# Kernel optimization log

Measured on AMD Instinct MI355X. Metric: run time of the kernel, lower is better.

## Reference

```python
import jax, jax.numpy as jnp
import numpy as np

N = 38333          # poi_len == number of graph nodes (forced by fc_layer input dim)
E = 38333 * 32     # edges, avg degree 32
VOCAB = 400 + 38333 + 1083   # cat_len + poi_len + user_len = 39816
EMB = (128 - 3) // 2         # 62
IN_DIM = EMB * 2 + 3         # 127
SLOPE = 0.01                 # LeakyReLU default negative_slope


def setup_inputs() -> dict:
    key = jax.random.key(0)
    ks = jax.random.split(key, 20)
    ids = jax.random.randint(ks[0], (N, 2), 0, VOCAB).astype(jnp.float32)
    feats = jax.random.uniform(ks[1], (N, 3), dtype=jnp.float32)
    x = jnp.concatenate([ids, feats], axis=1)                      # [N,5]
    edge_index = jax.random.randint(ks[2], (2, E), 0, N, dtype=jnp.int64)
    s = 0.05
    inp = {
        "x": x,
        "edge_index": edge_index,
        "emb": jax.random.normal(ks[3], (VOCAB, EMB), jnp.float32) * s,
        "W1": jax.random.normal(ks[4], (IN_DIM, 64), jnp.float32) * s,
        "b1": jnp.zeros((64,), jnp.float32),
        "W2": jax.random.normal(ks[5], (64, 32), jnp.float32) * s,
        "b2": jnp.zeros((32,), jnp.float32),
        "W3": jax.random.normal(ks[6], (32, 32), jnp.float32) * s,
        "b3": jnp.zeros((32,), jnp.float32),
        "W4": jax.random.normal(ks[7], (32, 32), jnp.float32) * s,
        "b4": jnp.zeros((32,), jnp.float32),
        "W5": jax.random.normal(ks[8], (32, 1), jnp.float32) * s,
        "b5": jnp.zeros((1,), jnp.float32),
        "Wf1": jax.random.normal(ks[9], (N, 128), jnp.float32) * s,
        "bf1": jnp.zeros((128,), jnp.float32),
        "Wf2": jax.random.normal(ks[10], (128, 128), jnp.float32) * s,
        "bf2": jnp.zeros((128,), jnp.float32),
    }
    return inp


def _forward(x, edge_index, emb, W1, b1, W2, b2, W3, b3, W4, b4, W5, b5, Wf1, bf1, Wf2, bf2):
    row, col = edge_index[0], edge_index[1]
    # GCN symmetric normalization with self-loops: deg includes the self-loop (+1)
    deg = jax.ops.segment_sum(jnp.ones((E,), x.dtype), col, num_segments=N) + 1.0
    dinv = jax.lax.rsqrt(deg)
    norm = dinv[row] * dinv[col]          # [E]
    self_norm = dinv * dinv               # [N]

    def gcn(h, W, b):
        hw = h @ W                         # [N,out]
        agg = jax.ops.segment_sum(hw[row] * norm[:, None], col, num_segments=N)
        return agg + hw * self_norm[:, None] + b

    lrelu = lambda z: jnp.where(z >= 0, z, SLOPE * z)

    ids = x[:, 0:2].astype(jnp.int32)
    h = jnp.concatenate([emb[ids].reshape(N, -1), x[:, 2:5]], axis=1)  # [N,127]
    h = lrelu(gcn(h, W1, b1))
    h = lrelu(gcn(h, W2, b2))
    t = gcn(h, W3, b3)
    h = lrelu(t) + t
    t = gcn(h, W4, b4)
    h = lrelu(t) + t
    h = lrelu(gcn(h, W5, b5))              # [N,1]
    v = h.reshape(-1)                      # [N] == poi_len
    o = jax.nn.relu(v @ Wf1 + bf1)
    o = jax.nn.relu(o @ Wf2 + bf2)
    return o


def reference(x, edge_index, emb, W1, b1, W2, b2, W3, b3, W4, b4, W5, b5, Wf1, bf1, Wf2, bf2):
    return _forward(x, edge_index, emb, W1, b1, W2, b2, W3, b3, W4, b4, W5, b5, Wf1, bf1, Wf2, bf2)
```

## Files before the change

kernel.cpp:

```cpp
#include <hip/hip_runtime.h>
#include <math.h>

#define SLOPE 0.01f
#define FC1_BLOCKS 512
#define NB 256
#define HBLK 256
#define BCHUNK 2048
#define X64SC 512.0f


static inline int cdiv_l(long a, int b) { return (int)((a + (long)b - 1) / (long)b); }

__device__ __forceinline__ unsigned short f2bf(float f) {
    union { float f; unsigned int i; } x; x.f = f;
    unsigned int i = x.i;
    i += 0x7fffu + ((i >> 16) & 1u);
    return (unsigned short)(i >> 16);
}
__device__ __forceinline__ float bf2f(unsigned short u) {
    union { unsigned int i; float f; } x; x.i = ((unsigned int)u) << 16;
    return x.f;
}
__device__ __forceinline__ float4 bf2f4(ushort4 u) {
    return make_float4(bf2f(u.x), bf2f(u.y), bf2f(u.z), bf2f(u.w));
}
__device__ __forceinline__ ushort4 f2bf4(float4 f) {
    return make_ushort4(f2bf(f.x), f2bf(f.y), f2bf(f.z), f2bf(f.w));
}

__device__ __forceinline__ float4 fp8x4_to_f4(unsigned int u) {
    auto lo = __builtin_amdgcn_cvt_pk_f32_fp8(u, false);
    auto hi = __builtin_amdgcn_cvt_pk_f32_fp8(u, true);
    return make_float4(lo[0], lo[1], hi[0], hi[1]);
}
__device__ __forceinline__ unsigned int f4_to_fp8x4(float4 v) {
    unsigned int u = 0;
    u = __builtin_amdgcn_cvt_pk_fp8_f32(v.x, v.y, u, false);
    u = __builtin_amdgcn_cvt_pk_fp8_f32(v.z, v.w, u, true);
    return u;
}

__global__ void k_front(const int* __restrict__ col, int* __restrict__ bhist, int E, int S,
                        const float* __restrict__ x, const float* __restrict__ emb,
                        unsigned short* __restrict__ h0, int N,
                        const float* __restrict__ W1, float* __restrict__ W1p,
                        int h0Blocks) {
    int b = blockIdx.x;
    if (b < HBLK) {
        __shared__ int hist[NB];
        int t = threadIdx.x;
        if (t < NB) hist[t] = 0;
        __syncthreads();
        for (int e = b * 256 + t; e < E; e += HBLK * 256)
            atomicAdd(&hist[col[e] / S], 1);
        __syncthreads();
        if (t < NB) bhist[b * NB + t] = hist[t];
        return;
    }
    b -= HBLK;
    if (b < h0Blocks) {
        int idx = b * 256 + threadIdx.x;
        if (idx >= N * 32) return;
        int i = idx >> 5;
        int g = idx & 31;
        const float* xr = x + (long)i * 5;
        int id0 = (int)xr[0], id1 = (int)xr[1];
        const float* e0p = emb + (long)id0 * 62;
        const float* e1p = emb + (long)id1 * 62;
        float v[4];
#pragma unroll
        for (int kk = 0; kk < 4; ++kk) {
            int k = 4 * g + kk;
            float val;
            if (k < 62)       val = e0p[k];
            else if (k < 124) val = e1p[k - 62];
            else if (k < 127) val = xr[2 + (k - 124)];
            else              val = 0.f;
            v[kk] = val;
        }
        *(ushort4*)(h0 + (long)i * 128 + 4 * g) =
            make_ushort4(f2bf(v[0]), f2bf(v[1]), f2bf(v[2]), f2bf(v[3]));
        return;
    }
    b -= h0Blocks;
    {
        int idx = b * 256 + threadIdx.x;
        if (idx >= 128 * 64) return;
        int k = idx >> 6;
        W1p[idx] = (k < 127) ? W1[idx] : 0.f;
    }
}

__global__ void k_bscan(const int* __restrict__ bhist, int* __restrict__ gcur,
                        int* __restrict__ gstart) {
    __shared__ int sums[4][NB];
    __shared__ int sc[NB];
    int t = threadIdx.x;
    int colId = t & (NB - 1), part = t >> 8;
    int s = 0;
    for (int b = part * (HBLK / 4); b < (part + 1) * (HBLK / 4); ++b)
        s += bhist[b * NB + colId];
    sums[part][colId] = s;
    __syncthreads();
    if (t < NB) {
        int v = sums[0][t] + sums[1][t] + sums[2][t] + sums[3][t];
        sc[t] = v;
    }
    __syncthreads();
    int v = (t < NB) ? sc[t] : 0;
    for (int d = 1; d < NB; d <<= 1) {
        int u = (t < NB && t >= d) ? sc[t - d] : 0;
        __syncthreads();
        if (t < NB) sc[t] += u;
        __syncthreads();
    }
    if (t < NB) {
        int excl = sc[t] - v;
        gcur[t] = excl;
        gstart[t] = excl;
        if (t == NB - 1) gstart[NB] = sc[t];
    }
}

__global__ void k_bucket(const int* __restrict__ row, const int* __restrict__ col,
                         int* __restrict__ gcur, unsigned int* __restrict__ ebuf,
                         int E, int S) {
    __shared__ int hist[NB], base[NB], lcur[NB];
    int t = threadIdx.x;
    if (t < NB) { hist[t] = 0; lcur[t] = 0; }
    __syncthreads();
    int e0 = blockIdx.x * BCHUNK;
    int e1 = min(e0 + BCHUNK, E);
    for (int e = e0 + t; e < e1; e += blockDim.x)
        atomicAdd(&hist[col[e] / S], 1);
    __syncthreads();
    if (t < NB) base[t] = hist[t] ? atomicAdd(&gcur[t], hist[t]) : 0;
    __syncthreads();
    for (int e = e0 + t; e < e1; e += blockDim.x) {
        int c = col[e], r = row[e];
        int b = c / S;
        int p = base[b] + atomicAdd(&lcur[b], 1);
        ebuf[p] = ((unsigned)c << 16) | (unsigned)r;
    }
}

__global__ void k_sortb(const unsigned int* __restrict__ ebuf,
                        const int* __restrict__ gstart,
                        int* __restrict__ off, float* __restrict__ dinv,
                        unsigned short* __restrict__ srcs, int N, int S, int E) {
    __shared__ int cntl[NB];
    __shared__ int lcur[NB];
    int b = blockIdx.x, t = threadIdx.x;
    int base_node = b * S;
    int nNodes = min(S, N - base_node);
    int start = gstart[b], end = gstart[b + 1];
    if (t < S) cntl[t] = 0;
    __syncthreads();
    for (int e = start + t; e < end; e += blockDim.x)
        atomicAdd(&cntl[(int)(ebuf[e] >> 16) - base_node], 1);
    __syncthreads();
    int myc = (t < S) ? cntl[t] : 0;
    for (int d = 1; d < S; d <<= 1) {
        int u = (t < S && t >= d) ? cntl[t - d] : 0;
        __syncthreads();
        if (t < S) cntl[t] += u;
        __syncthreads();
    }
    if (t < nNodes) {
        int excl = cntl[t] - myc;
        int node = base_node + t;
        off[node] = start + excl;
        dinv[node] = (float)(1.0 / sqrt((double)myc + 1.0));
        lcur[t] = excl;
    }
    if (b == NB - 1 && t == 0) off[N] = E;
    __syncthreads();
    for (int e = start + t; e < end; e += blockDim.x) {
        unsigned p = ebuf[e];
        int cl = (int)(p >> 16) - base_node;
        int pos = start + atomicAdd(&lcur[cl], 1);
        srcs[pos] = (unsigned short)(p & 0xFFFFu);
    }
}

__global__ void k_hw_rb8(const unsigned short* __restrict__ h, int ld,
                         const float* __restrict__ W,
                         const float* __restrict__ dinv, unsigned char* __restrict__ out,
                         int N) {
    constexpr int DIN = 128, DOUT = 64;
    constexpr int Q = DOUT / 4;
    int tid = blockIdx.x * blockDim.x + threadIdx.x;
    int G = (N + 3) >> 2;
    if (tid >= G * Q) return;
    int g = tid / Q;
    int q = tid % Q;
    int i0 = 4 * g;
    const ushort4* h0 = (const ushort4*)(h + (long)i0 * ld);
    const ushort4* h1 = (const ushort4*)(h + (long)(i0 + 1) * ld);
    const ushort4* h2 = (const ushort4*)(h + (long)(i0 + 2) * ld);
    const ushort4* h3 = (const ushort4*)(h + (long)(i0 + 3) * ld);
    const float* wp = W + 4 * q;
    float4 acc0 = make_float4(0.f, 0.f, 0.f, 0.f);
    float4 acc1 = acc0, acc2 = acc0, acc3 = acc0;
#pragma unroll 4
    for (int kk = 0; kk < DIN / 4; ++kk) {
        float4 a0 = bf2f4(h0[kk]), a1 = bf2f4(h1[kk]);
        float4 a2 = bf2f4(h2[kk]), a3 = bf2f4(h3[kk]);
        float4 w0 = *(const float4*)(wp + (long)(4 * kk)     * DOUT);
        float4 w1 = *(const float4*)(wp + (long)(4 * kk + 1) * DOUT);
        float4 w2 = *(const float4*)(wp + (long)(4 * kk + 2) * DOUT);
        float4 w3 = *(const float4*)(wp + (long)(4 * kk + 3) * DOUT);
        acc0.x += a0.x * w0.x + a0.y * w1.x + a0.z * w2.x + a0.w * w3.x;
        acc0.y += a0.x * w0.y + a0.y * w1.y + a0.z * w2.y + a0.w * w3.y;
        acc0.z += a0.x * w0.z + a0.y * w1.z + a0.z * w2.z + a0.w * w3.z;
        acc0.w += a0.x * w0.w + a0.y * w1.w + a0.z * w2.w + a0.w * w3.w;
        acc1.x += a1.x * w0.x + a1.y * w1.x + a1.z * w2.x + a1.w * w3.x;
        acc1.y += a1.x * w0.y + a1.y * w1.y + a1.z * w2.y + a1.w * w3.y;
        acc1.z += a1.x * w0.z + a1.y * w1.z + a1.z * w2.z + a1.w * w3.z;
        acc1.w += a1.x * w0.w + a1.y * w1.w + a1.z * w2.w + a1.w * w3.w;
        acc2.x += a2.x * w0.x + a2.y * w1.x + a2.z * w2.x + a2.w * w3.x;
        acc2.y += a2.x * w0.y + a2.y * w1.y + a2.z * w2.y + a2.w * w3.y;
        acc2.z += a2.x * w0.z + a2.y * w1.z + a2.z * w2.z + a2.w * w3.z;
        acc2.w += a2.x * w0.w + a2.y * w1.w + a2.z * w2.w + a2.w * w3.w;
        acc3.x += a3.x * w0.x + a3.y * w1.x + a3.z * w2.x + a3.w * w3.x;
        acc3.y += a3.x * w0.y + a3.y * w1.y + a3.z * w2.y + a3.w * w3.y;
        acc3.z += a3.x * w0.z + a3.y * w1.z + a3.z * w2.z + a3.w * w3.z;
        acc3.w += a3.x * w0.w + a3.y * w1.w + a3.z * w2.w + a3.w * w3.w;
    }
    float d0 = dinv[i0] * X64SC, d1 = dinv[i0 + 1] * X64SC;
    float d2 = dinv[i0 + 2] * X64SC, d3 = dinv[i0 + 3] * X64SC;
    acc0.x *= d0; acc0.y *= d0; acc0.z *= d0; acc0.w *= d0;
    acc1.x *= d1; acc1.y *= d1; acc1.z *= d1; acc1.w *= d1;
    acc2.x *= d2; acc2.y *= d2; acc2.z *= d2; acc2.w *= d2;
    acc3.x *= d3; acc3.y *= d3; acc3.z *= d3; acc3.w *= d3;
    unsigned char* op = out + (long)i0 * DOUT + 4 * q;
    *(unsigned int*)(op) = f4_to_fp8x4(acc0);
    if (i0 + 1 < N) *(unsigned int*)(op + DOUT)     = f4_to_fp8x4(acc1);
    if (i0 + 2 < N) *(unsigned int*)(op + 2 * DOUT) = f4_to_fp8x4(acc2);
    if (i0 + 3 < N) *(unsigned int*)(op + 3 * DOUT) = f4_to_fp8x4(acc3);
}

__global__ void k_fused64_fp8(const int* __restrict__ off,
                              const unsigned short* __restrict__ srcs,
                              const float* __restrict__ dinv,
                              const unsigned char* __restrict__ hin,
                              const float* __restrict__ bg,
                              const float* __restrict__ W,
                              unsigned short* __restrict__ hwsOut, int N) {
    constexpr int DG = 64, QG = 16, NPB = 16;
    __shared__ float hrow[NPB][DG + 4];
    int t = threadIdx.x;
    int n = t / QG, q = t % QG;
    int c = blockIdx.x * NPB + n;
    const unsigned int* hp = (const unsigned int*)hin;
    if (c < N) {
        int e0 = off[c], e1 = off[c + 1];
        float dc = dinv[c] * (1.0f / X64SC);
        float4 acc = fp8x4_to_f4(hp[((long)c << 4) + q]);
        int e = e0;
        for (; e + 7 < e1; e += 8) {
            int r0 = srcs[e],     r1 = srcs[e + 1], r2 = srcs[e + 2], r3 = srcs[e + 3];
            int r4 = srcs[e + 4], r5 = srcs[e + 5], r6 = srcs[e + 6], r7 = srcs[e + 7];
            float4 v0 = fp8x4_to_f4(hp[((long)r0 << 4) + q]);
            float4 v1 = fp8x4_to_f4(hp[((long)r1 << 4) + q]);
            float4 v2 = fp8x4_to_f4(hp[((long)r2 << 4) + q]);
            float4 v3 = fp8x4_to_f4(hp[((long)r3 << 4) + q]);
            float4 v4 = fp8x4_to_f4(hp[((long)r4 << 4) + q]);
            float4 v5 = fp8x4_to_f4(hp[((long)r5 << 4) + q]);
            float4 v6 = fp8x4_to_f4(hp[((long)r6 << 4) + q]);
            float4 v7 = fp8x4_to_f4(hp[((long)r7 << 4) + q]);
            acc.x += (v0.x + v1.x) + (v2.x + v3.x);
            acc.y += (v0.y + v1.y) + (v2.y + v3.y);
            acc.z += (v0.z + v1.z) + (v2.z + v3.z);
            acc.w += (v0.w + v1.w) + (v2.w + v3.w);
            acc.x += (v4.x + v5.x) + (v6.x + v7.x);
            acc.y += (v4.y + v5.y) + (v6.y + v7.y);
            acc.z += (v4.z + v5.z) + (v6.z + v7.z);
            acc.w += (v4.w + v5.w) + (v6.w + v7.w);
        }
        for (; e + 3 < e1; e += 4) {
            int r0 = srcs[e], r1 = srcs[e + 1], r2 = srcs[e + 2], r3 = srcs[e + 3];
            float4 v0 = fp8x4_to_f4(hp[((long)r0 << 4) + q]);
            float4 v1 = fp8x4_to_f4(hp[((long)r1 << 4) + q]);
            float4 v2 = fp8x4_to_f4(hp[((long)r2 << 4) + q]);
            float4 v3 = fp8x4_to_f4(hp[((long)r3 << 4) + q]);
            acc.x += (v0.x + v1.x) + (v2.x + v3.x);
            acc.y += (v0.y + v1.y) + (v2.y + v3.y);
            acc.z += (v0.z + v1.z) + (v2.z + v3.z);
            acc.w += (v0.w + v1.w) + (v2.w + v3.w);
        }
        for (; e < e1; ++e) {
            int r = srcs[e];
            float4 v = fp8x4_to_f4(hp[((long)r << 4) + q]);
            acc.x += v.x; acc.y += v.y; acc.z += v.z; acc.w += v.w;
        }
        float4 bb = *(const float4*)(bg + 4 * q);
        float t0 = acc.x * dc + bb.x, t1 = acc.y * dc + bb.y;
        float t2 = acc.z * dc + bb.z, t3 = acc.w * dc + bb.w;
        float4 res;
        res.x = (t0 >= 0.f) ? t0 : SLOPE * t0;
        res.y = (t1 >= 0.f) ? t1 : SLOPE * t1;
        res.z = (t2 >= 0.f) ? t2 : SLOPE * t2;
        res.w = (t3 >= 0.f) ? t3 : SLOPE * t3;
        *(float4*)&hrow[n][4 * q] = res;
    }
    __syncthreads();
    int n2 = t >> 3;
    int q2 = t & 7;
    if (n2 < NPB) {
        int c2 = blockIdx.x * NPB + n2;
        if (c2 < N) {
            const float* wp = W + 4 * q2;
            float4 acc = make_float4(0.f, 0.f, 0.f, 0.f);
#pragma unroll
            for (int kk = 0; kk < DG / 4; ++kk) {
                float4 a = *(const float4*)&hrow[n2][4 * kk];
                float4 w0 = *(const float4*)(wp + (long)(4 * kk)     * 32);
                float4 w1 = *(const float4*)(wp + (long)(4 * kk + 1) * 32);
                float4 w2 = *(const float4*)(wp + (long)(4 * kk + 2) * 32);
                float4 w3 = *(const float4*)(wp + (long)(4 * kk + 3) * 32);
                acc.x += a.x * w0.x + a.y * w1.x + a.z * w2.x + a.w * w3.x;
                acc.y += a.x * w0.y + a.y * w1.y + a.z * w2.y + a.w * w3.y;
                acc.z += a.x * w0.z + a.y * w1.z + a.z * w2.z + a.w * w3.z;
                acc.w += a.x * w0.w + a.y * w1.w + a.z * w2.w + a.w * w3.w;
            }
            float di = dinv[c2];
            acc.x *= di; acc.y *= di; acc.z *= di; acc.w *= di;
            *(ushort4*)(hwsOut + (long)c2 * 32 + 4 * q2) = f2bf4(acc);
        }
    }
}

template<int DG>
__global__ void k_fused(const int* __restrict__ off,
                        const unsigned short* __restrict__ srcs,
                        const float* __restrict__ dinv,
                        const unsigned short* __restrict__ hin,
                        const float* __restrict__ bg, int mode,
                        const float* __restrict__ W,
                        unsigned short* __restrict__ hwsOut, int N) {
    constexpr int QG = DG / 4;
    constexpr int NPB = 256 / QG;
    __shared__ float hrow[NPB][DG + 4];
    int t = threadIdx.x;
    int n = t / QG, q = t % QG;
    int c = blockIdx.x * NPB + n;
    if (c < N) {
        int e0 = off[c], e1 = off[c + 1];
        float dc = dinv[c];
        float4 acc = bf2f4(*(const ushort4*)(hin + (long)c * DG + 4 * q));
        int e = e0;
        for (; e + 7 < e1; e += 8) {
            int r0 = srcs[e],     r1 = srcs[e + 1], r2 = srcs[e + 2], r3 = srcs[e + 3];
            int r4 = srcs[e + 4], r5 = srcs[e + 5], r6 = srcs[e + 6], r7 = srcs[e + 7];
            float4 v0 = bf2f4(*(const ushort4*)(hin + (long)r0 * DG + 4 * q));
            float4 v1 = bf2f4(*(const ushort4*)(hin + (long)r1 * DG + 4 * q));
            float4 v2 = bf2f4(*(const ushort4*)(hin + (long)r2 * DG + 4 * q));
            float4 v3 = bf2f4(*(const ushort4*)(hin + (long)r3 * DG + 4 * q));
            float4 v4 = bf2f4(*(const ushort4*)(hin + (long)r4 * DG + 4 * q));
            float4 v5 = bf2f4(*(const ushort4*)(hin + (long)r5 * DG + 4 * q));
            float4 v6 = bf2f4(*(const ushort4*)(hin + (long)r6 * DG + 4 * q));
            float4 v7 = bf2f4(*(const ushort4*)(hin + (long)r7 * DG + 4 * q));
            acc.x += (v0.x + v1.x) + (v2.x + v3.x);
            acc.y += (v0.y + v1.y) + (v2.y + v3.y);
            acc.z += (v0.z + v1.z) + (v2.z + v3.z);
            acc.w += (v0.w + v1.w) + (v2.w + v3.w);
            acc.x += (v4.x + v5.x) + (v6.x + v7.x);
            acc.y += (v4.y + v5.y) + (v6.y + v7.y);
            acc.z += (v4.z + v5.z) + (v6.z + v7.z);
            acc.w += (v4.w + v5.w) + (v6.w + v7.w);
        }
        for (; e + 3 < e1; e += 4) {
            int r0 = srcs[e], r1 = srcs[e + 1], r2 = srcs[e + 2], r3 = srcs[e + 3];
            float4 v0 = bf2f4(*(const ushort4*)(hin + (long)r0 * DG + 4 * q));
            float4 v1 = bf2f4(*(const ushort4*)(hin + (long)r1 * DG + 4 * q));
            float4 v2 = bf2f4(*(const ushort4*)(hin + (long)r2 * DG + 4 * q));
            float4 v3 = bf2f4(*(const ushort4*)(hin + (long)r3 * DG + 4 * q));
            acc.x += (v0.x + v1.x) + (v2.x + v3.x);
            acc.y += (v0.y + v1.y) + (v2.y + v3.y);
            acc.z += (v0.z + v1.z) + (v2.z + v3.z);
            acc.w += (v0.w + v1.w) + (v2.w + v3.w);
        }
        for (; e < e1; ++e) {
            int r = srcs[e];
            float4 v = bf2f4(*(const ushort4*)(hin + (long)r * DG + 4 * q));
            acc.x += v.x; acc.y += v.y; acc.z += v.z; acc.w += v.w;
        }
        float4 bb = *(const float4*)(bg + 4 * q);
        float t0 = acc.x * dc + bb.x, t1 = acc.y * dc + bb.y;
        float t2 = acc.z * dc + bb.z, t3 = acc.w * dc + bb.w;
        float4 res;
        if (mode == 0) {
            res.x = (t0 >= 0.f) ? t0 : SLOPE * t0;
            res.y = (t1 >= 0.f) ? t1 : SLOPE * t1;
            res.z = (t2 >= 0.f) ? t2 : SLOPE * t2;
            res.w = (t3 >= 0.f) ? t3 : SLOPE * t3;
        } else {
            res.x = (t0 >= 0.f) ? 2.f * t0 : (1.f + SLOPE) * t0;
            res.y = (t1 >= 0.f) ? 2.f * t1 : (1.f + SLOPE) * t1;
            res.z = (t2 >= 0.f) ? 2.f * t2 : (1.f + SLOPE) * t2;
            res.w = (t3 >= 0.f) ? 2.f * t3 : (1.f + SLOPE) * t3;
        }
        *(float4*)&hrow[n][4 * q] = res;
    }
    __syncthreads();
    int n2 = t >> 3;
    int q2 = t & 7;
    if (n2 < NPB) {
        int c2 = blockIdx.x * NPB + n2;
        if (c2 < N) {
            const float* wp = W + 4 * q2;
            float4 acc = make_float4(0.f, 0.f, 0.f, 0.f);
#pragma unroll
            for (int kk = 0; kk < DG / 4; ++kk) {
                float4 a = *(const float4*)&hrow[n2][4 * kk];
                float4 w0 = *(const float4*)(wp + (long)(4 * kk)     * 32);
                float4 w1 = *(const float4*)(wp + (long)(4 * kk + 1) * 32);
                float4 w2 = *(const float4*)(wp + (long)(4 * kk + 2) * 32);
                float4 w3 = *(const float4*)(wp + (long)(4 * kk + 3) * 32);
                acc.x += a.x * w0.x + a.y * w1.x + a.z * w2.x + a.w * w3.x;
                acc.y += a.x * w0.y + a.y * w1.y + a.z * w2.y + a.w * w3.y;
                acc.z += a.x * w0.z + a.y * w1.z + a.z * w2.z + a.w * w3.z;
                acc.w += a.x * w0.w + a.y * w1.w + a.z * w2.w + a.w * w3.w;
            }
            float di = dinv[c2];
            acc.x *= di; acc.y *= di; acc.z *= di; acc.w *= di;
            *(ushort4*)(hwsOut + (long)c2 * 32 + 4 * q2) = f2bf4(acc);
        }
    }
}

__global__ void k_fused_last(const int* __restrict__ off,
                             const unsigned short* __restrict__ srcs,
                             const float* __restrict__ dinv,
                             const unsigned short* __restrict__ hin,
                             const float* __restrict__ bg,
                             const float* __restrict__ W5,
                             float* __restrict__ hwsOut, int N) {
    constexpr int QG = 8;
    constexpr int NPB = 32;
    __shared__ float hrow[NPB][36];
    int t = threadIdx.x;
    int n = t / QG, q = t % QG;
    int c = blockIdx.x * NPB + n;
    if (c < N) {
        int e0 = off[c], e1 = off[c + 1];
        float dc = dinv[c];
        float4 acc = bf2f4(*(const ushort4*)(hin + (long)c * 32 + 4 * q));
        int e = e0;
        for (; e + 7 < e1; e += 8) {
            int r0 = srcs[e],     r1 = srcs[e + 1], r2 = srcs[e + 2], r3 = srcs[e + 3];
            int r4 = srcs[e + 4], r5 = srcs[e + 5], r6 = srcs[e + 6], r7 = srcs[e + 7];
            float4 v0 = bf2f4(*(const ushort4*)(hin + (long)r0 * 32 + 4 * q));
            float4 v1 = bf2f4(*(const ushort4*)(hin + (long)r1 * 32 + 4 * q));
            float4 v2 = bf2f4(*(const ushort4*)(hin + (long)r2 * 32 + 4 * q));
            float4 v3 = bf2f4(*(const ushort4*)(hin + (long)r3 * 32 + 4 * q));
            float4 v4 = bf2f4(*(const ushort4*)(hin + (long)r4 * 32 + 4 * q));
            float4 v5 = bf2f4(*(const ushort4*)(hin + (long)r5 * 32 + 4 * q));
            float4 v6 = bf2f4(*(const ushort4*)(hin + (long)r6 * 32 + 4 * q));
            float4 v7 = bf2f4(*(const ushort4*)(hin + (long)r7 * 32 + 4 * q));
            acc.x += (v0.x + v1.x) + (v2.x + v3.x);
            acc.y += (v0.y + v1.y) + (v2.y + v3.y);
            acc.z += (v0.z + v1.z) + (v2.z + v3.z);
            acc.w += (v0.w + v1.w) + (v2.w + v3.w);
            acc.x += (v4.x + v5.x) + (v6.x + v7.x);
            acc.y += (v4.y + v5.y) + (v6.y + v7.y);
            acc.z += (v4.z + v5.z) + (v6.z + v7.z);
            acc.w += (v4.w + v5.w) + (v6.w + v7.w);
        }
        for (; e + 3 < e1; e += 4) {
            int r0 = srcs[e], r1 = srcs[e + 1], r2 = srcs[e + 2], r3 = srcs[e + 3];
            float4 v0 = bf2f4(*(const ushort4*)(hin + (long)r0 * 32 + 4 * q));
            float4 v1 = bf2f4(*(const ushort4*)(hin + (long)r1 * 32 + 4 * q));
            float4 v2 = bf2f4(*(const ushort4*)(hin + (long)r2 * 32 + 4 * q));
            float4 v3 = bf2f4(*(const ushort4*)(hin + (long)r3 * 32 + 4 * q));
            acc.x += (v0.x + v1.x) + (v2.x + v3.x);
            acc.y += (v0.y + v1.y) + (v2.y + v3.y);
            acc.z += (v0.z + v1.z) + (v2.z + v3.z);
            acc.w += (v0.w + v1.w) + (v2.w + v3.w);
        }
        for (; e < e1; ++e) {
            int r = srcs[e];
            float4 v = bf2f4(*(const ushort4*)(hin + (long)r * 32 + 4 * q));
            acc.x += v.x; acc.y += v.y; acc.z += v.z; acc.w += v.w;
        }
        float4 bb = *(const float4*)(bg + 4 * q);
        float t0 = acc.x * dc + bb.x, t1 = acc.y * dc + bb.y;
        float t2 = acc.z * dc + bb.z, t3 = acc.w * dc + bb.w;
        float4 res;
        res.x = (t0 >= 0.f) ? 2.f * t0 : (1.f + SLOPE) * t0;
        res.y = (t1 >= 0.f) ? 2.f * t1 : (1.f + SLOPE) * t1;
        res.z = (t2 >= 0.f) ? 2.f * t2 : (1.f + SLOPE) * t2;
        res.w = (t3 >= 0.f) ? 2.f * t3 : (1.f + SLOPE) * t3;
        *(float4*)&hrow[n][4 * q] = res;
    }
    __syncthreads();
    if (t < NPB) {
        int c2 = blockIdx.x * NPB + t;
        if (c2 < N) {
            float acc = 0.f;
#pragma unroll
            for (int kk = 0; kk < 8; ++kk) {
                float4 a = *(const float4*)&hrow[t][4 * kk];
                acc += a.x * W5[4 * kk] + a.y * W5[4 * kk + 1]
                     + a.z * W5[4 * kk + 2] + a.w * W5[4 * kk + 3];
            }
            hwsOut[c2] = acc * dinv[c2];
        }
    }
}

__global__ void k_tail(const int* __restrict__ off,
                       const unsigned short* __restrict__ srcs,
                       const float* __restrict__ dinv, const float* __restrict__ hws,
                       const float* __restrict__ b5,
                       const float* __restrict__ Wf1, double* __restrict__ part,
                       int N, int chunk) {
    __shared__ float Vl[96];
    int bl = blockIdx.x, t = threadIdx.x;
    int i0 = bl * chunk;
    int i1 = min(i0 + chunk, N);
    int cnt = i1 - i0;
    if (t < cnt) {
        int c = i0 + t;
        int e0 = off[c], e1 = off[c + 1];
        float acc = hws[c];
        float a1 = 0.f, a2 = 0.f, a3 = 0.f;
        int e = e0;
        for (; e + 3 < e1; e += 4) {
            acc += hws[srcs[e]];
            a1  += hws[srcs[e + 1]];
            a2  += hws[srcs[e + 2]];
            a3  += hws[srcs[e + 3]];
        }
        for (; e < e1; ++e) acc += hws[srcs[e]];
        float tt = (acc + a1 + a2 + a3) * dinv[c] + b5[0];
        Vl[t] = (tt >= 0.f) ? tt : SLOPE * tt;
    }
    __syncthreads();
    int j = t;
    double a0 = 0.0, a1 = 0.0, a2 = 0.0, a3 = 0.0;
    int i = 0;
    for (; i + 3 < cnt; i += 4) {
        a0 += (double)Vl[i]     * (double)Wf1[(long)(i0 + i)     * 128 + j];
        a1 += (double)Vl[i + 1] * (double)Wf1[(long)(i0 + i + 1) * 128 + j];
        a2 += (double)Vl[i + 2] * (double)Wf1[(long)(i0 + i + 2) * 128 + j];
        a3 += (double)Vl[i + 3] * (double)Wf1[(long)(i0 + i + 3) * 128 + j];
    }
    for (; i < cnt; ++i)
        a0 += (double)Vl[i] * (double)Wf1[(long)(i0 + i) * 128 + j];
    part[bl * 128 + j] = (a0 + a1) + (a2 + a3);
}

__global__ void k_fc1b(const double* __restrict__ part, const float* __restrict__ bf1,
                       float* __restrict__ o1) {
    __shared__ double red[256];
    int j = blockIdx.x;
    int t = threadIdx.x;
    double a = part[t * 128 + j] + part[(t + 256) * 128 + j];
    red[t] = a;
    __syncthreads();
    for (int s = 128; s > 0; s >>= 1) {
        if (t < s) red[t] += red[t + s];
        __syncthreads();
    }
    if (t == 0) {
        double v = red[0] + (double)bf1[j];
        o1[j] = (float)((v > 0.0) ? v : 0.0);
    }
}

__global__ void k_fc2(const float* __restrict__ o1, const float* __restrict__ Wf2,
                      const float* __restrict__ bf2, float* __restrict__ out) {
    __shared__ double red[128];
    int j = blockIdx.x;
    int k = threadIdx.x;
    red[k] = (double)o1[k] * (double)Wf2[(long)k * 128 + j];
    __syncthreads();
    for (int s = 64; s > 0; s >>= 1) {
        if (k < s) red[k] += red[k + s];
        __syncthreads();
    }
    if (k == 0) {
        double u = red[0] + (double)bf2[j];
        out[j] = (float)((u > 0.0) ? u : 0.0);
    }
}

extern "C" void kernel_launch(void* const* d_in, const int* in_sizes, int n_in,
                              void* d_out, int out_size, void* d_ws, size_t ws_size,
                              hipStream_t stream) {
    const float* x   = (const float*)d_in[0];
    const int*   ei  = (const int*)d_in[1];
    const float* emb = (const float*)d_in[2];
    const float* W1  = (const float*)d_in[3];
    const float* b1  = (const float*)d_in[4];
    const float* W2  = (const float*)d_in[5];
    const float* b2  = (const float*)d_in[6];
    const float* W3  = (const float*)d_in[7];
    const float* b3  = (const float*)d_in[8];
    const float* W4  = (const float*)d_in[9];
    const float* b4  = (const float*)d_in[10];
    const float* W5  = (const float*)d_in[11];
    const float* b5  = (const float*)d_in[12];
    const float* Wf1 = (const float*)d_in[13];
    const float* bf1 = (const float*)d_in[14];
    const float* Wf2 = (const float*)d_in[15];
    const float* bf2 = (const float*)d_in[16];

    const int N = in_sizes[0] / 5;
    const int E = in_sizes[1] / 2;
    const int* row = ei;
    const int* col = ei + E;
    const int S = (N + NB - 1) / NB;
    const int Np = N + 4;

    char* ws = (char*)d_ws;
    size_t off_b = 0;
    auto alloc = [&](size_t bytes) -> void* {
        void* p = ws + off_b;
        off_b += (bytes + 255) & ~(size_t)255;
        return p;
    };
    int*   offcsr = (int*)alloc((size_t)(N + 1) * sizeof(int));
    int*   bhist  = (int*)alloc((size_t)HBLK * NB * sizeof(int));
    int*   gcur   = (int*)alloc((size_t)NB * sizeof(int));
    int*   gstart = (int*)alloc((size_t)(NB + 1) * sizeof(int));
    unsigned short* srcs = (unsigned short*)alloc((size_t)E * sizeof(unsigned short));
    unsigned int* ebuf = (unsigned int*)alloc((size_t)E * sizeof(unsigned int));
    float* dinv   = (float*)alloc((size_t)Np * sizeof(float));
    float* W1p    = (float*)alloc((size_t)128 * 64 * sizeof(float));
    unsigned short* H0   = (unsigned short*)alloc((size_t)Np * 128 * sizeof(unsigned short));
    unsigned char*  X64f8 = (unsigned char*)alloc((size_t)Np * 64 * sizeof(unsigned char));
    unsigned short* X32a = (unsigned short*)alloc((size_t)Np * 32 * sizeof(unsigned short));
    unsigned short* X32b = (unsigned short*)alloc((size_t)Np * 32 * sizeof(unsigned short));
    unsigned short* X32c = (unsigned short*)alloc((size_t)Np * 32 * sizeof(unsigned short));
    float* HWSf   = (float*)alloc((size_t)Np * sizeof(float));
    double* part  = (double*)alloc((size_t)FC1_BLOCKS * 128 * sizeof(double));
    float* O1     = (float*)alloc(128 * sizeof(float));

    int h0Blocks  = cdiv_l((long)N * 32, 256);
    int padBlocks = cdiv_l(128 * 64, 256);
    k_front<<<HBLK + h0Blocks + padBlocks, 256, 0, stream>>>(
        col, bhist, E, S, x, emb, H0, N, W1, W1p, h0Blocks);

    k_bscan<<<1, 1024, 0, stream>>>(bhist, gcur, gstart);
    k_bucket<<<cdiv_l(E, BCHUNK), 256, 0, stream>>>(row, col, gcur, ebuf, E, S);
    k_sortb<<<NB, 1024, 0, stream>>>(ebuf, gstart, offcsr, dinv, srcs, N, S, E);

    {
        int G = (N + 3) / 4;
        k_hw_rb8<<<cdiv_l((long)G * 16, 256), 256, 0, stream>>>(
            H0, 128, W1p, dinv, X64f8, N);
    }
    k_fused64_fp8<<<cdiv_l(N, 16), 256, 0, stream>>>(
        offcsr, srcs, dinv, X64f8, b1, W2, X32a, N);
    k_fused<32><<<cdiv_l(N, 32), 256, 0, stream>>>(
        offcsr, srcs, dinv, X32a, b2, 0, W3, X32b, N);
    k_fused<32><<<cdiv_l(N, 32), 256, 0, stream>>>(
        offcsr, srcs, dinv, X32b, b3, 1, W4, X32c, N);
    k_fused_last<<<cdiv_l(N, 32), 256, 0, stream>>>(
        offcsr, srcs, dinv, X32c, b4, W5, HWSf, N);

    int chunk = (N + FC1_BLOCKS - 1) / FC1_BLOCKS;
    k_tail<<<FC1_BLOCKS, 128, 0, stream>>>(
        offcsr, srcs, dinv, HWSf, b5, Wf1, part, N, chunk);
    k_fc1b<<<128, 256, 0, stream>>>(part, bf1, O1);
    k_fc2<<<128, 128, 0, stream>>>(O1, Wf2, bf2, (float*)d_out);
}
```

Before: 263.2 us.

## Store 32-wide GCN layer activations as per-row-scaled int8 instead of bf16

The intermediate 32-channel node features for layers 2–4 are quantized to int8 with a per-row absmax scale stored in a separate float array, replacing bf16 storage. The gather-aggregate kernels dequantize each neighbor row with its scale, halving the bytes gathered per edge. In exchange, every edge now needs an extra scale load, the 8-way unrolled inner loop is dropped in favour of a 4-way one, and int8 precision adds quantization error.

```diff
diff --git a/kernel.cpp b/kernel.cpp
--- a/kernel.cpp
+++ b/kernel.cpp
@@ -6,7 +6,7 @@
 #define NB 256
 #define HBLK 256
 #define BCHUNK 2048
-#define X64SC 512.0f
+#define F8SC 512.0f
 
 
 static inline int cdiv_l(long a, int b) { return (int)((a + (long)b - 1) / (long)b); }
@@ -38,6 +38,19 @@
     u = __builtin_amdgcn_cvt_pk_fp8_f32(v.x, v.y, u, false);
     u = __builtin_amdgcn_cvt_pk_fp8_f32(v.z, v.w, u, true);
     return u;
+}
+
+__device__ __forceinline__ float4 i8x4_to_f4(unsigned int u) {
+    return make_float4((float)(signed char)(u & 0xffu),
+                       (float)(signed char)((u >> 8) & 0xffu),
+                       (float)(signed char)((u >> 16) & 0xffu),
+                       (float)(signed char)((u >> 24) & 0xffu));
+}
+__device__ __forceinline__ unsigned int f4_to_i8x4(float4 v, float inv) {
+    int qx = __float2int_rn(v.x * inv), qy = __float2int_rn(v.y * inv);
+    int qz = __float2int_rn(v.z * inv), qw = __float2int_rn(v.w * inv);
+    return (unsigned)(qx & 0xff) | ((unsigned)(qy & 0xff) << 8) |
+           ((unsigned)(qz & 0xff) << 16) | ((unsigned)(qw & 0xff) << 24);
 }
 
 __global__ void k_front(const int* __restrict__ col, int* __restrict__ bhist, int E, int S,
@@ -227,8 +240,8 @@
         acc3.z += a3.x * w0.z + a3.y * w1.z + a3.z * w2.z + a3.w * w3.z;
         acc3.w += a3.x * w0.w + a3.y * w1.w + a3.z * w2.w + a3.w * w3.w;
     }
-    float d0 = dinv[i0] * X64SC, d1 = dinv[i0 + 1] * X64SC;
-    float d2 = dinv[i0 + 2] * X64SC, d3 = dinv[i0 + 3] * X64SC;
+    float d0 = dinv[i0] * F8SC, d1 = dinv[i0 + 1] * F8SC;
+    float d2 = dinv[i0 + 2] * F8SC, d3 = dinv[i0 + 3] * F8SC;
     acc0.x *= d0; acc0.y *= d0; acc0.z *= d0; acc0.w *= d0;
     acc1.x *= d1; acc1.y *= d1; acc1.z *= d1; acc1.w *= d1;
     acc2.x *= d2; acc2.y *= d2; acc2.z *= d2; acc2.w *= d2;
@@ -246,7 +259,8 @@
                               const unsigned char* __restrict__ hin,
                               const float* __restrict__ bg,
                               const float* __restrict__ W,
-                              unsigned short* __restrict__ hwsOut, int N) {
+                              unsigned char* __restrict__ hwsOut,
+                              float* __restrict__ sclOut, int N) {
     constexpr int DG = 64, QG = 16, NPB = 16;
     __shared__ float hrow[NPB][DG + 4];
     int t = threadIdx.x;
@@ -255,7 +269,7 @@
     const unsigned int* hp = (const unsigned int*)hin;
     if (c < N) {
         int e0 = off[c], e1 = off[c + 1];
-        float dc = dinv[c] * (1.0f / X64SC);
+        float dc = dinv[c] * (1.0f / F8SC);
         float4 acc = fp8x4_to_f4(hp[((long)c << 4) + q]);
         int e = e0;
         for (; e + 7 < e1; e += 8) {
@@ -326,65 +340,56 @@
             }
             float di = dinv[c2];
             acc.x *= di; acc.y *= di; acc.z *= di; acc.w *= di;
-            *(ushort4*)(hwsOut + (long)c2 * 32 + 4 * q2) = f2bf4(acc);
-        }
-    }
-}
-
-template<int DG>
-__global__ void k_fused(const int* __restrict__ off,
-                        const unsigned short* __restrict__ srcs,
-                        const float* __restrict__ dinv,
-                        const unsigned short* __restrict__ hin,
-                        const float* __restrict__ bg, int mode,
-                        const float* __restrict__ W,
-                        unsigned short* __restrict__ hwsOut, int N) {
-    constexpr int QG = DG / 4;
-    constexpr int NPB = 256 / QG;
+            float lm = fmaxf(fmaxf(fabsf(acc.x), fabsf(acc.y)),
+                             fmaxf(fabsf(acc.z), fabsf(acc.w)));
+#pragma unroll
+            for (int m = 1; m < 8; m <<= 1) lm = fmaxf(lm, __shfl_xor(lm, m));
+            float inv = (lm > 0.f) ? 127.f / lm : 0.f;
+            *(unsigned int*)(hwsOut + (long)c2 * 32 + 4 * q2) = f4_to_i8x4(acc, inv);
+            if (q2 == 0) sclOut[c2] = lm * (1.f / 127.f);
+        }
+    }
+}
+
+__global__ void k_fused32_i8(const int* __restrict__ off,
+                             const unsigned short* __restrict__ srcs,
+                             const float* __restrict__ dinv,
+                             const unsigned char* __restrict__ hin,
+                             const float* __restrict__ sclIn,
+                             const float* __restrict__ bg, int mode,
+                             const float* __restrict__ W,
+                             unsigned char* __restrict__ hwsOut,
+                             float* __restrict__ sclOut, int N) {
+    constexpr int DG = 32, QG = 8, NPB = 32;
     __shared__ float hrow[NPB][DG + 4];
     int t = threadIdx.x;
     int n = t / QG, q = t % QG;
     int c = blockIdx.x * NPB + n;
+    const unsigned int* hp = (const unsigned int*)hin;
     if (c < N) {
         int e0 = off[c], e1 = off[c + 1];
         float dc = dinv[c];
-        float4 acc = bf2f4(*(const ushort4*)(hin + (long)c * DG + 4 * q));
+        float s0 = sclIn[c];
+        float4 sv = i8x4_to_f4(hp[((long)c << 3) + q]);
+        float4 acc = make_float4(sv.x * s0, sv.y * s0, sv.z * s0, sv.w * s0);
         int e = e0;
-        for (; e + 7 < e1; e += 8) {
-            int r0 = srcs[e],     r1 = srcs[e + 1], r2 = srcs[e + 2], r3 = srcs[e + 3];
-            int r4 = srcs[e + 4], r5 = srcs[e + 5], r6 = srcs[e + 6], r7 = srcs[e + 7];
-            float4 v0 = bf2f4(*(const ushort4*)(hin + (long)r0 * DG + 4 * q));
-            float4 v1 = bf2f4(*(const ushort4*)(hin + (long)r1 * DG + 4 * q));
-            float4 v2 = bf2f4(*(const ushort4*)(hin + (long)r2 * DG + 4 * q));
-            float4 v3 = bf2f4(*(const ushort4*)(hin + (long)r3 * DG + 4 * q));
-            float4 v4 = bf2f4(*(const ushort4*)(hin + (long)r4 * DG + 4 * q));
-            float4 v5 = bf2f4(*(const ushort4*)(hin + (long)r5 * DG + 4 * q));
-            float4 v6 = bf2f4(*(const ushort4*)(hin + (long)r6 * DG + 4 * q));
-            float4 v7 = bf2f4(*(const ushort4*)(hin + (long)r7 * DG + 4 * q));
-            acc.x += (v0.x + v1.x) + (v2.x + v3.x);
-            acc.y += (v0.y + v1.y) + (v2.y + v3.y);
-            acc.z += (v0.z + v1.z) + (v2.z + v3.z);
-            acc.w += (v0.w + v1.w) + (v2.w + v3.w);
-            acc.x += (v4.x + v5.x) + (v6.x + v7.x);
-            acc.y += (v4.y + v5.y) + (v6.y + v7.y);
-            acc.z += (v4.z + v5.z) + (v6.z + v7.z);
-            acc.w += (v4.w + v5.w) + (v6.w + v7.w);
-        }
         for (; e + 3 < e1; e += 4) {
             int r0 = srcs[e], r1 = srcs[e + 1], r2 = srcs[e + 2], r3 = srcs[e + 3];
-            float4 v0 = bf2f4(*(const ushort4*)(hin + (long)r0 * DG + 4 * q));
-            float4 v1 = bf2f4(*(const ushort4*)(hin + (long)r1 * DG + 4 * q));
-            float4 v2 = bf2f4(*(const ushort4*)(hin + (long)r2 * DG + 4 * q));
-            float4 v3 = bf2f4(*(const ushort4*)(hin + (long)r3 * DG + 4 * q));
-            acc.x += (v0.x + v1.x) + (v2.x + v3.x);
-            acc.y += (v0.y + v1.y) + (v2.y + v3.y);
-            acc.z += (v0.z + v1.z) + (v2.z + v3.z);
-            acc.w += (v0.w + v1.w) + (v2.w + v3.w);
+            float sa = sclIn[r0], sb = sclIn[r1], sc2 = sclIn[r2], sd = sclIn[r3];
+            float4 v0 = i8x4_to_f4(hp[((long)r0 << 3) + q]);
+            float4 v1 = i8x4_to_f4(hp[((long)r1 << 3) + q]);
+            float4 v2 = i8x4_to_f4(hp[((long)r2 << 3) + q]);
+            float4 v3 = i8x4_to_f4(hp[((long)r3 << 3) + q]);
+            acc.x += v0.x * sa + v1.x * sb + v2.x * sc2 + v3.x * sd;
+            acc.y += v0.y * sa + v1.y * sb + v2.y * sc2 + v3.y * sd;
+            acc.z += v0.z * sa + v1.z * sb + v2.z * sc2 + v3.z * sd;
+            acc.w += v0.w * sa + v1.w * sb + v2.w * sc2 + v3.w * sd;
         }
         for (; e < e1; ++e) {
             int r = srcs[e];
-            float4 v = bf2f4(*(const ushort4*)(hin + (long)r * DG + 4 * q));
-            acc.x += v.x; acc.y += v.y; acc.z += v.z; acc.w += v.w;
+            float s = sclIn[r];
+            float4 v = i8x4_to_f4(hp[((long)r << 3) + q]);
+            acc.x += v.x * s; acc.y += v.y * s; acc.z += v.z * s; acc.w += v.w * s;
         }
         float4 bb = *(const float4*)(bg + 4 * q);
         float t0 = acc.x * dc + bb.x, t1 = acc.y * dc + bb.y;
@@ -406,7 +411,7 @@
     __syncthreads();
     int n2 = t >> 3;
     int q2 = t & 7;
-    if (n2 < NPB) {
+    {
         int c2 = blockIdx.x * NPB + n2;
         if (c2 < N) {
             const float* wp = W + 4 * q2;
@@ -425,64 +430,56 @@
             }
             float di = dinv[c2];
             acc.x *= di; acc.y *= di; acc.z *= di; acc.w *= di;
-            *(ushort4*)(hwsOut + (long)c2 * 32 + 4 * q2) = f2bf4(acc);
-        }
-    }
-}
-
-__global__ void k_fused_last(const int* __restrict__ off,
-                             const unsigned short* __restrict__ srcs,
-                             const float* __restrict__ dinv,
-                             const unsigned short* __restrict__ hin,
-                             const float* __restrict__ bg,
-                             const float* __restrict__ W5,
-                             float* __restrict__ hwsOut, int N) {
+            float lm = fmaxf(fmaxf(fabsf(acc.x), fabsf(acc.y)),
+                             fmaxf(fabsf(acc.z), fabsf(acc.w)));
+#pragma unroll
+            for (int m = 1; m < 8; m <<= 1) lm = fmaxf(lm, __shfl_xor(lm, m));
+            float inv = (lm > 0.f) ? 127.f / lm : 0.f;
+            *(unsigned int*)(hwsOut + (long)c2 * 32 + 4 * q2) = f4_to_i8x4(acc, inv);
+            if (q2 == 0) sclOut[c2] = lm * (1.f / 127.f);
+        }
+    }
+}
+
+__global__ void k_fused_last_i8(const int* __restrict__ off,
+                                const unsigned short* __restrict__ srcs,
+                                const float* __restrict__ dinv,
+                                const unsigned char* __restrict__ hin,
+                                const float* __restrict__ sclIn,
+                                const float* __restrict__ bg,
+                                const float* __restrict__ W5,
+                                float* __restrict__ hwsOut, int N) {
     constexpr int QG = 8;
     constexpr int NPB = 32;
     __shared__ float hrow[NPB][36];
     int t = threadIdx.x;
     int n = t / QG, q = t % QG;
     int c = blockIdx.x * NPB + n;
+    const unsigned int* hp = (const unsigned int*)hin;
     if (c < N) {
         int e0 = off[c], e1 = off[c + 1];
         float dc = dinv[c];
-        float4 acc = bf2f4(*(const ushort4*)(hin + (long)c * 32 + 4 * q));
+        float s0 = sclIn[c];
+        float4 sv = i8x4_to_f4(hp[((long)c << 3) + q]);
+        float4 acc = make_float4(sv.x * s0, sv.y * s0, sv.z * s0, sv.w * s0);
         int e = e0;
-        for (; e + 7 < e1; e += 8) {
-            int r0 = srcs[e],     r1 = srcs[e + 1], r2 = srcs[e + 2], r3 = srcs[e + 3];
-            int r4 = srcs[e + 4], r5 = srcs[e + 5], r6 = srcs[e + 6], r7 = srcs[e + 7];
-            float4 v0 = bf2f4(*(const ushort4*)(hin + (long)r0 * 32 + 4 * q));
-            float4 v1 = bf2f4(*(const ushort4*)(hin + (long)r1 * 32 + 4 * q));
-            float4 v2 = bf2f4(*(const ushort4*)(hin + (long)r2 * 32 + 4 * q));
-            float4 v3 = bf2f4(*(const ushort4*)(hin + (long)r3 * 32 + 4 * q));
-            float4 v4 = bf2f4(*(const ushort4*)(hin + (long)r4 * 32 + 4 * q));
-            float4 v5 = bf2f4(*(const ushort4*)(hin + (long)r5 * 32 + 4 * q));
-            float4 v6 = bf2f4(*(const ushort4*)(hin + (long)r6 * 32 + 4 * q));
-            float4 v7 = bf2f4(*(const ushort4*)(hin + (long)r7 * 32 + 4 * q));
-            acc.x += (v0.x + v1.x) + (v2.x + v3.x);
-            acc.y += (v0.y + v1.y) + (v2.y + v3.y);
-            acc.z += (v0.z + v1.z) + (v2.z + v3.z);
-            acc.w += (v0.w + v1.w) + (v2.w + v3.w);
-            acc.x += (v4.x + v5.x) + (v6.x + v7.x);
-            acc.y += (v4.y + v5.y) + (v6.y + v7.y);
-            acc.z += (v4.z + v5.z) + (v6.z + v7.z);
-            acc.w += (v4.w + v5.w) + (v6.w + v7.w);
-        }
         for (; e + 3 < e1; e += 4) {
             int r0 = srcs[e], r1 = srcs[e + 1], r2 = srcs[e + 2], r3 = srcs[e + 3];
-            float4 v0 = bf2f4(*(const ushort4*)(hin + (long)r0 * 32 + 4 * q));
-            float4 v1 = bf2f4(*(const ushort4*)(hin + (long)r1 * 32 + 4 * q));
-            float4 v2 = bf2f4(*(const ushort4*)(hin + (long)r2 * 32 + 4 * q));
-            float4 v3 = bf2f4(*(const ushort4*)(hin + (long)r3 * 32 + 4 * q));
-            acc.x += (v0.x + v1.x) + (v2.x + v3.x);
-            acc.y += (v0.y + v1.y) + (v2.y + v3.y);
-            acc.z += (v0.z + v1.z) + (v2.z + v3.z);
-            acc.w += (v0.w + v1.w) + (v2.w + v3.w);
+            float sa = sclIn[r0], sb = sclIn[r1], sc2 = sclIn[r2], sd = sclIn[r3];
+            float4 v0 = i8x4_to_f4(hp[((long)r0 << 3) + q]);
+            float4 v1 = i8x4_to_f4(hp[((long)r1 << 3) + q]);
+            float4 v2 = i8x4_to_f4(hp[((long)r2 << 3) + q]);
+            float4 v3 = i8x4_to_f4(hp[((long)r3 << 3) + q]);
+            acc.x += v0.x * sa + v1.x * sb + v2.x * sc2 + v3.x * sd;
+            acc.y += v0.y * sa + v1.y * sb + v2.y * sc2 + v3.y * sd;
+            acc.z += v0.z * sa + v1.z * sb + v2.z * sc2 + v3.z * sd;
+            acc.w += v0.w * sa + v1.w * sb + v2.w * sc2 + v3.w * sd;
         }
         for (; e < e1; ++e) {
             int r = srcs[e];
-            float4 v = bf2f4(*(const ushort4*)(hin + (long)r * 32 + 4 * q));
-            acc.x += v.x; acc.y += v.y; acc.z += v.z; acc.w += v.w;
+            float s = sclIn[r];
+            float4 v = i8x4_to_f4(hp[((long)r << 3) + q]);
+            acc.x += v.x * s; acc.y += v.y * s; acc.z += v.z * s; acc.w += v.w * s;
         }
         float4 bb = *(const float4*)(bg + 4 * q);
         float t0 = acc.x * dc + bb.x, t1 = acc.y * dc + bb.y;
@@ -632,9 +629,12 @@
     float* W1p    = (float*)alloc((size_t)128 * 64 * sizeof(float));
     unsigned short* H0   = (unsigned short*)alloc((size_t)Np * 128 * sizeof(unsigned short));
     unsigned char*  X64f8 = (unsigned char*)alloc((size_t)Np * 64 * sizeof(unsigned char));
-    unsigned short* X32a = (unsigned short*)alloc((size_t)Np * 32 * sizeof(unsigned short));
-    unsigned short* X32b = (unsigned short*)alloc((size_t)Np * 32 * sizeof(unsigned short));
-    unsigned short* X32c = (unsigned short*)alloc((size_t)Np * 32 * sizeof(unsigned short));
+    unsigned char*  X32a = (unsigned char*)alloc((size_t)Np * 32 * sizeof(unsigned char));
+    unsigned char*  X32b = (unsigned char*)alloc((size_t)Np * 32 * sizeof(unsigned char));
+    unsigned char*  X32c = (unsigned char*)alloc((size_t)Np * 32 * sizeof(unsigned char));
+    float* sclA   = (float*)alloc((size_t)Np * sizeof(float));
+    float* sclB   = (float*)alloc((size_t)Np * sizeof(float));
+    float* sclC   = (float*)alloc((size_t)Np * sizeof(float));
     float* HWSf   = (float*)alloc((size_t)Np * sizeof(float));
     double* part  = (double*)alloc((size_t)FC1_BLOCKS * 128 * sizeof(double));
     float* O1     = (float*)alloc(128 * sizeof(float));
@@ -654,13 +654,13 @@
             H0, 128, W1p, dinv, X64f8, N);
     }
     k_fused64_fp8<<<cdiv_l(N, 16), 256, 0, stream>>>(
-        offcsr, srcs, dinv, X64f8, b1, W2, X32a, N);
-    k_fused<32><<<cdiv_l(N, 32), 256, 0, stream>>>(
-        offcsr, srcs, dinv, X32a, b2, 0, W3, X32b, N);
-    k_fused<32><<<cdiv_l(N, 32), 256, 0, stream>>>(
-        offcsr, srcs, dinv, X32b, b3, 1, W4, X32c, N);
-    k_fused_last<<<cdiv_l(N, 32), 256, 0, stream>>>(
-        offcsr, srcs, dinv, X32c, b4, W5, HWSf, N);
+        offcsr, srcs, dinv, X64f8, b1, W2, X32a, sclA, N);
+    k_fused32_i8<<<cdiv_l(N, 32), 256, 0, stream>>>(
+        offcsr, srcs, dinv, X32a, sclA, b2, 0, W3, X32b, sclB, N);
+    k_fused32_i8<<<cdiv_l(N, 32), 256, 0, stream>>>(
+        offcsr, srcs, dinv, X32b, sclB, b3, 1, W4, X32c, sclC, N);
+    k_fused_last_i8<<<cdiv_l(N, 32), 256, 0, stream>>>(
+        offcsr, srcs, dinv, X32c, sclC, b4, W5, HWSf, N);
 
     int chunk = (N + FC1_BLOCKS - 1) / FC1_BLOCKS;
     k_tail<<<FC1_BLOCKS, 128, 0, stream>>>(
```

New measurement: 272.8 us. 1.04x slower.
